# Kernel tuning notes

Measured on AMD Instinct MI355X. Metric: run time of the kernel, lower is better.

## Reference

```python
import jax, jax.numpy as jnp
import numpy as np

H = 50  # hidden size (hardcoded in the torch module)

def lstm_cell(h, c, xt, Wih, Whh, bih, bhh):
    # xt: [B, D]; gates packed PyTorch-style: i, f, g, o each of size H
    gates = xt @ Wih.T + h @ Whh.T + bih + bhh  # [B, 4H]
    i, f, g, o = jnp.split(gates, 4, axis=-1)
    i = jax.nn.sigmoid(i)
    f = jax.nn.sigmoid(f)
    g = jnp.tanh(g)
    o = jax.nn.sigmoid(o)
    c_new = f * c + i * g
    h_new = o * jnp.tanh(c_new)
    return h_new, c_new

def lstm_last_hidden(x, Wih, Whh, bih, bhh):
    # x: [B, T, D] -> final hidden state h_T: [B, H] (zero init state)
    B = x.shape[0]
    h0 = jnp.zeros((B, H), dtype=x.dtype)
    c0 = jnp.zeros((B, H), dtype=x.dtype)
    def step(carry, xt):
        h, c = carry
        h, c = lstm_cell(h, c, xt, Wih, Whh, bih, bhh)
        return (h, c), None
    (hT, _), _ = jax.lax.scan(step, (h0, c0), jnp.swapaxes(x, 0, 1))
    return hT

def setup_inputs() -> dict:
    key = jax.random.key(0)
    ks = jax.random.split(key, 11)
    s = 1.0 / np.sqrt(H)  # PyTorch LSTM/Linear init scale
    u = lambda k, shape: jax.random.uniform(k, shape, jnp.float32, -s, s)
    return {
        'x': jax.random.normal(ks[0], (2048, 1024, 1), jnp.float32),
        'lstm1_Wih': u(ks[1], (4 * H, 1)),
        'lstm1_Whh': u(ks[2], (4 * H, H)),
        'lstm1_bih': u(ks[3], (4 * H,)),
        'lstm1_bhh': u(ks[4], (4 * H,)),
        'lstm2_Wih': u(ks[5], (4 * H, H)),
        'lstm2_Whh': u(ks[6], (4 * H, H)),
        'lstm2_bih': u(ks[7], (4 * H,)),
        'lstm2_bhh': u(ks[8], (4 * H,)),
        'fc_W': u(ks[9], (1, H)),
        'fc_b': u(ks[10], (1,)),
    }

def reference(x, lstm1_Wih, lstm1_Whh, lstm1_bih, lstm1_bhh,
              lstm2_Wih, lstm2_Whh, lstm2_bih, lstm2_bhh, fc_W, fc_b):
    # lstm1 over full sequence; only the last timestep output is used downstream
    h1 = lstm_last_hidden(x, lstm1_Wih, lstm1_Whh, lstm1_bih, lstm1_bhh)  # [B, H]
    # lstm2 sees a length-1 sequence starting from zero state -> one cell step
    B = x.shape[0]
    z = jnp.zeros((B, H), dtype=x.dtype)
    h2, _ = lstm_cell(z, z, h1, lstm2_Wih, lstm2_Whh, lstm2_bih, lstm2_bhh)  # [B, H]
    return h2 @ fc_W.T + fc_b  # [B, 1]
```

## Files before the change

kernel.cpp:

```cpp
#include <hip/hip_runtime.h>

#define HH 50
#define TT 1024
#define BT 8
#define NB (2048 / BT)
#define CHUNK 256
#define XST 260
#define HST 72

typedef _Float16 half8 __attribute__((ext_vector_type(8)));
typedef float f32x4 __attribute__((ext_vector_type(4)));

union H8 { half8 v; _Float16 h[8]; unsigned short u[8]; unsigned int i[4]; };

__device__ __forceinline__ float rcp_f(float x) { return __builtin_amdgcn_rcpf(x); }

#if __has_builtin(__builtin_amdgcn_exp2f)
__device__ __forceinline__ float exp2_f(float x) { return __builtin_amdgcn_exp2f(x); }
#else
__device__ __forceinline__ float exp2_f(float x) { return __expf(0.6931471805599453f * x); }
#endif

#define L2E   1.4426950408889634f
#define L2E2  2.8853900817779268f

__device__ __forceinline__ float sigm_n(float a) {
    return rcp_f(1.0f + exp2_f(a));
}
__device__ __forceinline__ float tanh_p(float a) {
    return __builtin_fmaf(-2.0f, rcp_f(1.0f + exp2_f(a)), 1.0f);
}
__device__ __forceinline__ unsigned short f2h(float f) {
    return __builtin_bit_cast(unsigned short, (_Float16)f);
}
__device__ __forceinline__ float bperm(int addr, float v) {
    return __builtin_bit_cast(float,
        __builtin_amdgcn_ds_bpermute(addr, __builtin_bit_cast(int, v)));
}

__global__ __launch_bounds__(512) void lstm_mfma_kernel(
    const float* __restrict__ x,
    const float* __restrict__ wih1, const float* __restrict__ whh1,
    const float* __restrict__ bih1, const float* __restrict__ bhh1,
    const float* __restrict__ wih2,
    const float* __restrict__ bih2, const float* __restrict__ bhh2,
    const float* __restrict__ fcw,  const float* __restrict__ fcb,
    float* __restrict__ out)
{
    __shared__ float xs[BT * XST];
    __shared__ __align__(16) unsigned short hb[2][16 * HST];
    __shared__ float h2s[BT * 52];

    const int tid  = threadIdx.x;
    const int wv   = tid >> 6;
    const int js   = wv & 3;
    const int bh   = wv >> 2;
    const int lane = tid & 63;
    const int l16  = lane & 15;
    const int quad = lane >> 4;
    const int j    = js * 16 + l16;
    const bool jv  = (j < HH);
    const bool q2  = (quad == 2);
    const int b0   = blockIdx.x * BT;
    const int  srcl  = ((quad >> 1) * 16 + l16) * 4;
    const bool qodd  = (quad & 1);
    const bool useb1 = (((quad ^ (quad >> 1)) & 1) == 0);
    const int  bmine = quad * 2 + bh;

    H8 bw[4][2];
    #pragma unroll
    for (int t4 = 0; t4 < 4; ++t4) {
        const float sc = (t4 == 2) ? L2E2 : -L2E;
        const int row = t4 * HH + j;
        #pragma unroll
        for (int kk = 0; kk < 2; ++kk)
            #pragma unroll
            for (int e = 0; e < 8; ++e) {
                const int k = kk * 32 + quad * 8 + e;
                const float v = (jv && k < HH) ? whh1[row * HH + k] * sc : 0.0f;
                bw[t4][kk].h[e] = (_Float16)v;
            }
        if (q2) {
            const float bsc = jv ? (bih1[row] + bhh1[row]) * sc : 0.0f;
            const _Float16 bhi = (_Float16)bsc;
            bw[t4][1].h[2] = (_Float16)(jv ? wih1[row] * sc : 0.0f);
            bw[t4][1].h[3] = bhi;
            bw[t4][1].h[4] = (_Float16)(bsc - (float)bhi);
        }
    }

    for (int i = tid; i < 2 * 16 * HST; i += 512) {
        const int col = i % HST;
        ((unsigned short*)hb)[i] = (col == 51 || col == 52) ? 0x3c00 : 0;
    }

    float c = 0.f;
    const f32x4 kZ = {0.f, 0.f, 0.f, 0.f};
    const bool xw = (wv == 0) && (lane < BT);

    auto cell = [&](float ai, float af, float ag, float ao, float& cc) -> unsigned short {
        const float Ei = exp2_f(ai), Ef = exp2_f(af), Eg = exp2_f(ag), Eo = exp2_f(ao);
        const float pf  = 1.0f + Ef;
        const float P   = (1.0f + Ei) * (1.0f + Eg);
        const float den = pf * P;
        const float num = __builtin_fmaf(cc, P, (Eg - 1.0f) * pf);
        cc = num * rcp_f(den);
        const float ac = fminf(cc * L2E2, 80.0f);
        const float Ec = exp2_f(ac);
        const float h  = (Ec - 1.0f) * rcp_f((1.0f + Eo) * (1.0f + Ec));
        return f2h(h);
    };

#define REDIST(G, PG)                                                                  \
    {                                                                                  \
        const float e00 = bh ? acc[G][1] : acc[G][0];                                  \
        const float e02 = bh ? acc[G][3] : acc[G][2];                                  \
        const float v1  = qodd ? e02 : e00;                                            \
        const float v2  = qodd ? e00 : e02;                                            \
        const float r1  = bperm(srcl, v1);                                             \
        const float r2  = bperm(srcl, v2);                                             \
        PG = useb1 ? r1 : r2;                                                          \
    }

#define STEP(T, CUR, NXT, STAGEOK)                                                     \
    {                                                                                  \
        const int tc = (T) & (CHUNK - 1);                                              \
        if (STAGEOK && tc == 0) {                                                      \
            {                       \
                const int r = tid >> 6, c4 = tid & 63;                                 \
                const float4 q = ((const float4*)x)[((b0 + r) * TT + (T)) / 4 + c4];   \
                *(float4*)&xs[r * XST + c4 * 4] = q;                                   \
            }                                                                          \
            __syncthreads();                    \
        }                                                                              \
        H8 a0, a1;                                                                     \
        a0.v = *(const half8*)&(CUR)[l16 * HST + quad * 8];                            \
        a1.v = *(const half8*)&(CUR)[l16 * HST + 32 + quad * 8];                       \
        if (STAGEOK && tc == 0) {                                                      \
             \
            const float xv = (l16 < BT) ? xs[l16 * XST] : 0.0f;                        \
            const unsigned int pk = 0x3c000000u | (unsigned int)f2h(xv);               \
            a1.i[1] = q2 ? pk : a1.i[1];                                               \
            a1.i[2] = q2 ? 0x00003c00u : a1.i[2];                                      \
        }                                                                              \
        float xnext = 0.0f;                                                            \
        if (xw) xnext = xs[lane * XST + ((tc + 1) & (CHUNK - 1))];                     \
        f32x4 acc[4];                                                                  \
        _Pragma("unroll")                                                              \
        for (int t4 = 0; t4 < 4; ++t4) {                                               \
            acc[t4] = __builtin_amdgcn_mfma_f32_16x16x32_f16(a0.v, bw[t4][0].v, kZ, 0, 0, 0);       \
            acc[t4] = __builtin_amdgcn_mfma_f32_16x16x32_f16(a1.v, bw[t4][1].v, acc[t4], 0, 0, 0);  \
        }                                                                              \
        float p0, p1, p2, p3;                                                          \
        REDIST(0, p0) REDIST(1, p1) REDIST(2, p2) REDIST(3, p3)                        \
        const unsigned short hv = cell(p0, p1, p2, p3, c);                             \
        if (jv) (NXT)[bmine * HST + j] = hv;    \
        if (xw) (NXT)[lane * HST + 50] = f2h(xnext);  \
        __syncthreads();                                                               \
    }

    for (int t = 0; t < TT; t += 2) {
        STEP(t,     hb[0], hb[1], true);
        STEP(t + 1, hb[1], hb[0], false);
    }
#undef STEP
#undef REDIST
    unsigned short* cur = hb[0];

    if (bh == 0) {
        H8 bw2[4][2];
        float b2[4];
        #pragma unroll
        for (int t4 = 0; t4 < 4; ++t4) {
            const float sc = (t4 == 2) ? L2E2 : -L2E;
            const int row = t4 * HH + j;
            #pragma unroll
            for (int kk = 0; kk < 2; ++kk)
                #pragma unroll
                for (int e = 0; e < 8; ++e) {
                    const int k = kk * 32 + quad * 8 + e;
                    const float v = (jv && k < HH) ? wih2[row * HH + k] * sc : 0.0f;
                    bw2[t4][kk].h[e] = (_Float16)v;
                }
            b2[t4] = jv ? (bih2[row] + bhh2[row]) * sc : 0.0f;
        }
        H8 a0, a1;
        a0.v = *(const half8*)&cur[l16 * HST + quad * 8];
        a1.v = *(const half8*)&cur[l16 * HST + 32 + quad * 8];
        f32x4 acc2[4];
        #pragma unroll
        for (int t4 = 0; t4 < 4; ++t4) {
            const f32x4 cb = {b2[t4], b2[t4], b2[t4], b2[t4]};
            acc2[t4] = __builtin_amdgcn_mfma_f32_16x16x32_f16(a0.v, bw2[t4][0].v, cb, 0, 0, 0);
            acc2[t4] = __builtin_amdgcn_mfma_f32_16x16x32_f16(a1.v, bw2[t4][1].v, acc2[t4], 0, 0, 0);
        }
        #pragma unroll
        for (int r = 0; r < 4; ++r) {
            const int b = quad * 4 + r;
            const float ig = sigm_n(acc2[0][r]);
            const float gg = tanh_p(acc2[2][r]);
            const float og = sigm_n(acc2[3][r]);
            const float cc = ig * gg;
            const float h2 = og * tanh_p(cc * L2E2);
            if (b < BT && jv) h2s[b * 52 + j] = h2;
        }
    }
    __syncthreads();

    if (tid < BT * 16) {
        const int b = tid >> 4, l = tid & 15;
        float p = 0.f;
        for (int jj = l; jj < HH; jj += 16)
            p = __builtin_fmaf(h2s[b * 52 + jj], fcw[jj], p);
        #pragma unroll
        for (int off = 8; off > 0; off >>= 1) p += __shfl_xor(p, off, 16);
        if (l == 0) out[b0 + b] = p + fcb[0];
    }
}

extern "C" void kernel_launch(void* const* d_in, const int* in_sizes, int n_in,
                              void* d_out, int out_size, void* d_ws, size_t ws_size,
                              hipStream_t stream) {
    lstm_mfma_kernel<<<NB, 512, 0, stream>>>(
        (const float*)d_in[0],
        (const float*)d_in[1], (const float*)d_in[2],
        (const float*)d_in[3], (const float*)d_in[4],
        (const float*)d_in[5],
        (const float*)d_in[7], (const float*)d_in[8],
        (const float*)d_in[9], (const float*)d_in[10],
        (float*)d_out);
}
```

Before: 516.8 us.

## Halve block to 4 waves, each computing two batch rows per lane

The block shrinks from 8 waves to 4. Previously the same MFMA was duplicated across two wave halves that each handled half the batch rows. Now each wave keeps both batch-row results from its MFMA output and evaluates two LSTM cells per lane, with a simpler bpermute redistribution. This removes redundant MFMA work and lowers the barrier cost per step. In exchange, each lane does twice the serial transcendental work on the critical path, and fewer waves are available to hide latency.

```diff
diff --git a/kernel.cpp b/kernel.cpp
--- a/kernel.cpp
+++ b/kernel.cpp
@@ -38,7 +38,7 @@
         __builtin_amdgcn_ds_bpermute(addr, __builtin_bit_cast(int, v)));
 }
 
-__global__ __launch_bounds__(512) void lstm_mfma_kernel(
+__global__ __launch_bounds__(256) void lstm_mfma_kernel(
     const float* __restrict__ x,
     const float* __restrict__ wih1, const float* __restrict__ whh1,
     const float* __restrict__ bih1, const float* __restrict__ bhh1,
@@ -53,8 +53,7 @@
 
     const int tid  = threadIdx.x;
     const int wv   = tid >> 6;
-    const int js   = wv & 3;
-    const int bh   = wv >> 2;
+    const int js   = wv;
     const int lane = tid & 63;
     const int l16  = lane & 15;
     const int quad = lane >> 4;
@@ -62,10 +61,9 @@
     const bool jv  = (j < HH);
     const bool q2  = (quad == 2);
     const int b0   = blockIdx.x * BT;
-    const int  srcl  = ((quad >> 1) * 16 + l16) * 4;
-    const bool qodd  = (quad & 1);
-    const bool useb1 = (((quad ^ (quad >> 1)) & 1) == 0);
-    const int  bmine = quad * 2 + bh;
+    const int  srcl  = (((quad & 1) << 4) + l16) * 4;
+    const bool qlow  = (quad < 2);
+    const int  bm0   = ((quad & 1) << 2) + ((quad >> 1) << 1);
 
     H8 bw[4][2];
     #pragma unroll
@@ -89,12 +87,12 @@
         }
     }
 
-    for (int i = tid; i < 2 * 16 * HST; i += 512) {
+    for (int i = tid; i < 2 * 16 * HST; i += 256) {
         const int col = i % HST;
         ((unsigned short*)hb)[i] = (col == 51 || col == 52) ? 0x3c00 : 0;
     }
 
-    float c = 0.f;
+    float c0 = 0.f, c1 = 0.f;
     const f32x4 kZ = {0.f, 0.f, 0.f, 0.f};
     const bool xw = (wv == 0) && (lane < BT);
 
@@ -111,23 +109,20 @@
         return f2h(h);
     };
 
-#define REDIST(G, PG)                                                                  \
+#define REDIST(G, P0, P1)                                                              \
     {                                                                                  \
-        const float e00 = bh ? acc[G][1] : acc[G][0];                                  \
-        const float e02 = bh ? acc[G][3] : acc[G][2];                                  \
-        const float v1  = qodd ? e02 : e00;                                            \
-        const float v2  = qodd ? e00 : e02;                                            \
-        const float r1  = bperm(srcl, v1);                                             \
-        const float r2  = bperm(srcl, v2);                                             \
-        PG = useb1 ? r1 : r2;                                                          \
+        const float r1 = bperm(srcl, acc[G][2]);                                       \
+        const float r2 = bperm(srcl, acc[G][3]);                                       \
+        P0 = qlow ? acc[G][0] : r1;                                                    \
+        P1 = qlow ? acc[G][1] : r2;                                                    \
     }
 
 #define STEP(T, CUR, NXT, STAGEOK)                                                     \
     {                                                                                  \
         const int tc = (T) & (CHUNK - 1);                                              \
         if (STAGEOK && tc == 0) {                                                      \
-            {                       \
-                const int r = tid >> 6, c4 = tid & 63;                                 \
+            for (int i = tid; i < BT * (CHUNK / 4); i += 256) {                        \
+                const int r = i >> 6, c4 = i & 63;                                     \
                 const float4 q = ((const float4*)x)[((b0 + r) * TT + (T)) / 4 + c4];   \
                 *(float4*)&xs[r * XST + c4 * 4] = q;                                   \
             }                                                                          \
@@ -151,10 +146,15 @@
             acc[t4] = __builtin_amdgcn_mfma_f32_16x16x32_f16(a0.v, bw[t4][0].v, kZ, 0, 0, 0);       \
             acc[t4] = __builtin_amdgcn_mfma_f32_16x16x32_f16(a1.v, bw[t4][1].v, acc[t4], 0, 0, 0);  \
         }                                                                              \
-        float p0, p1, p2, p3;                                                          \
-        REDIST(0, p0) REDIST(1, p1) REDIST(2, p2) REDIST(3, p3)                        \
-        const unsigned short hv = cell(p0, p1, p2, p3, c);                             \
-        if (jv) (NXT)[bmine * HST + j] = hv;    \
+        float pi0, pi1, pf0, pf1, pg0, pg1, po0, po1;                                  \
+        REDIST(0, pi0, pi1) REDIST(1, pf0, pf1)                                        \
+        REDIST(2, pg0, pg1) REDIST(3, po0, po1)                                        \
+        const unsigned short h0 = cell(pi0, pf0, pg0, po0, c0);                        \
+        const unsigned short h1 = cell(pi1, pf1, pg1, po1, c1);                        \
+        if (jv) {                \
+            (NXT)[bm0 * HST + j]       = h0;                                           \
+            (NXT)[(bm0 + 1) * HST + j] = h1;                                           \
+        }                                                                              \
         if (xw) (NXT)[lane * HST + 50] = f2h(xnext);  \
         __syncthreads();                                                               \
     }
@@ -167,7 +167,7 @@
 #undef REDIST
     unsigned short* cur = hb[0];
 
-    if (bh == 0) {
+    {
         H8 bw2[4][2];
         float b2[4];
         #pragma unroll
@@ -221,7 +221,7 @@
 extern "C" void kernel_launch(void* const* d_in, const int* in_sizes, int n_in,
                               void* d_out, int out_size, void* d_ws, size_t ws_size,
                               hipStream_t stream) {
-    lstm_mfma_kernel<<<NB, 512, 0, stream>>>(
+    lstm_mfma_kernel<<<NB, 256, 0, stream>>>(
         (const float*)d_in[0],
         (const float*)d_in[1], (const float*)d_in[2],
         (const float*)d_in[3], (const float*)d_in[4],
```

Result: no change. 507.7 us (-1.8%).
